# Kernel optimization log

Measured on AMD Instinct MI355X. Metric: run time of the kernel, lower is better.

The kernel has to match this reference:

```python
import jax, jax.numpy as jnp
import numpy as np

EPS = 1e-12  # torch F.normalize eps

def _normalize(x):
    n = jnp.sqrt(jnp.sum(x * x, axis=-1, keepdims=True))
    return x / jnp.maximum(n, EPS)

def bgs_extended(d6s):
    # d6s: [B, N, D, 3, 2] -> rotation [B, N, D, 3, 3] (columns b1,b2,b3)
    b1 = _normalize(d6s[..., :, 0])
    a2 = d6s[..., :, 1]
    dot = jnp.sum(b1 * a2, axis=-1, keepdims=True)
    b2 = _normalize(a2 - dot * b1)
    b3 = jnp.cross(b1, b2, axis=-1)
    return jnp.stack([b1, b2, b3], axis=-1)

def setup_inputs() -> dict:
    key = jax.random.key(0)
    k1, k2, k3, k4, k5 = jax.random.split(key, 5)
    B, N, D, F = 8, 8192, 64, 64
    X = jax.random.normal(k1, (B, N, D, 3), dtype=jnp.float32)
    J = jax.random.normal(k2, (B, N, D, 3, 2), dtype=jnp.float32)
    A = jax.random.normal(k3, (F, D), dtype=jnp.float32)
    Bm = jax.random.normal(k4, (F, D), dtype=jnp.float32)
    C = jax.random.normal(k5, (F, D), dtype=jnp.float32)
    return {"X": X, "J": J, "A": A, "Bm": Bm, "C": C}

def reference(X, J, A, Bm, C):
    R = bgs_extended(J)  # [B,N,D,3,3]
    # RT_i X = dot(column i of R, X) -> compute all three at once: [B,N,D,3]
    RTX = jnp.einsum('bndki,bndk->bndi', R, X)
    rt0, rt1, rt2 = RTX[..., 0:1], RTX[..., 1:2], RTX[..., 2:3]
    # get_rrtx(i, R, s) == R[..., :, i] * s
    a_term = R[..., :, 0] * rt0 + R[..., :, 1] * rt1
    b_term = R[..., :, 1] * rt0 - R[..., :, 0] * rt1
    c_term = R[..., :, 2] * rt2
    Y = (jnp.einsum('fe,bnei->bnfi', A, a_term)
         + jnp.einsum('fe,bnei->bnfi', Bm, b_term)
         + jnp.einsum('fe,bnei->bnfi', C, c_term))
    return Y
```

## Files before the change

kernel.cpp:

```cpp
#include <hip/hip_runtime.h>

typedef __bf16 bf16;
typedef bf16 bf16x8 __attribute__((ext_vector_type(8)));
typedef float f32x4 __attribute__((ext_vector_type(4)));
typedef unsigned int u32;

#define PTS 16
#define WREG 9216

__device__ __forceinline__ void gld_lds16(const void* g, void* l) {
    __builtin_amdgcn_global_load_lds(
        (const __attribute__((address_space(1))) u32*)g,
        (__attribute__((address_space(3))) u32*)l, 16, 0, 0);
}

__global__ __launch_bounds__(256, 4)
void affine_linear_fused(const float* __restrict__ X, const float* __restrict__ J,
                         const float* __restrict__ A, const float* __restrict__ Bm,
                         const float* __restrict__ C, float* __restrict__ Y)
{
    __shared__ __attribute__((aligned(128))) unsigned char lds[4 * WREG];

    const int tid  = threadIdx.x;
    const int wave = tid >> 6;
    const int lane = tid & 63;
    const int l16  = lane & 15;
    const int lq   = lane >> 4;
    const long bn0 = (long)blockIdx.x * PTS;

    unsigned char* wbase = &lds[wave * WREG];

    {
        const float* jg = J + (bn0 + wave * 4) * 64 * 6;
        const float* xg = X + (bn0 + wave * 4) * 64 * 3;
        #pragma unroll
        for (int t = 0; t < 6; ++t)
            gld_lds16(jg + t * 256 + lane * 4, wbase + t * 1024);
        #pragma unroll
        for (int t = 0; t < 3; ++t)
            gld_lds16(xg + t * 256 + lane * 4, wbase + 6144 + t * 1024);
    }

    const int f = wave * 16 + l16;
    bf16x8 wfrag[6];
    #pragma unroll
    for (int kk = 0; kk < 6; ++kk) {
        const float* src = (kk < 2) ? A : (kk < 4) ? Bm : C;
        const f32x4* p4 = (const f32x4*)(src + f * 64 + (kk & 1) * 32 + lq * 8);
        f32x4 lo = p4[0], hi = p4[1];
        bf16x8 w;
        w[0] = (bf16)lo[0]; w[1] = (bf16)lo[1]; w[2] = (bf16)lo[2]; w[3] = (bf16)lo[3];
        w[4] = (bf16)hi[0]; w[5] = (bf16)hi[1]; w[6] = (bf16)hi[2]; w[7] = (bf16)hi[3];
        wfrag[kk] = w;
    }

    __asm__ volatile("s_waitcnt vmcnt(0)" ::: "memory");

    const float* jlds = (const float*)wbase;
    const float* xlds = (const float*)(wbase + 6144);
    float jv[4][6], xv[4][3];
    #pragma unroll
    for (int q = 0; q < 4; ++q) {
        const float* jp = jlds + q * 384 + lane * 6;
        float2 ja = *(const float2*)(jp + 0);
        float2 jb = *(const float2*)(jp + 2);
        float2 jc = *(const float2*)(jp + 4);
        jv[q][0] = ja.x; jv[q][1] = ja.y;
        jv[q][2] = jb.x; jv[q][3] = jb.y;
        jv[q][4] = jc.x; jv[q][5] = jc.y;
        const float* xp = xlds + q * 192 + lane * 3;
        xv[q][0] = xp[0]; xv[q][1] = xp[1]; xv[q][2] = xp[2];
    }

    #pragma unroll
    for (int q = 0; q < 4; ++q) {
        float a1x = jv[q][0], a2x = jv[q][1];
        float a1y = jv[q][2], a2y = jv[q][3];
        float a1z = jv[q][4], a2z = jv[q][5];
        float xx = xv[q][0], xy = xv[q][1], xz = xv[q][2];

        float n1   = sqrtf(a1x*a1x + a1y*a1y + a1z*a1z);
        float inv1 = 1.0f / fmaxf(n1, 1e-12f);
        float b1x = a1x*inv1, b1y = a1y*inv1, b1z = a1z*inv1;
        float dot = b1x*a2x + b1y*a2y + b1z*a2z;
        float ux = a2x - dot*b1x, uy = a2y - dot*b1y, uz = a2z - dot*b1z;
        float n2   = sqrtf(ux*ux + uy*uy + uz*uz);
        float inv2 = 1.0f / fmaxf(n2, 1e-12f);
        float b2x = ux*inv2, b2y = uy*inv2, b2z = uz*inv2;
        float b3x = b1y*b2z - b1z*b2y;
        float b3y = b1z*b2x - b1x*b2z;
        float b3z = b1x*b2y - b1y*b2x;

        float rt0 = b1x*xx + b1y*xy + b1z*xz;
        float rt1 = b2x*xx + b2y*xy + b2z*xz;
        float rt2 = b3x*xx + b3y*xy + b3z*xz;

        float at0 = b1x*rt0 + b2x*rt1;
        float at1 = b1y*rt0 + b2y*rt1;
        float at2 = b1z*rt0 + b2z*rt1;
        float bt0 = b2x*rt0 - b1x*rt1;
        float bt1 = b2y*rt0 - b1y*rt1;
        float bt2 = b2z*rt0 - b1z*rt1;
        float ct0 = b3x*rt2, ct1 = b3y*rt2, ct2 = b3z*rt2;

        bf16* r0 = (bf16*)(wbase + (q*3 + 0) * 400);
        bf16* r1 = (bf16*)(wbase + (q*3 + 1) * 400);
        bf16* r2 = (bf16*)(wbase + (q*3 + 2) * 400);
        r0[lane] = (bf16)at0; r0[64+lane] = (bf16)bt0; r0[128+lane] = (bf16)ct0;
        r1[lane] = (bf16)at1; r1[64+lane] = (bf16)bt1; r1[128+lane] = (bf16)ct1;
        r2[lane] = (bf16)at2; r2[64+lane] = (bf16)bt2; r2[128+lane] = (bf16)ct2;
    }
    __syncthreads();

    f32x4 acc[3];
    #pragma unroll
    for (int mt = 0; mt < 3; ++mt) {
        int m  = mt * 16 + l16;
        int wv = m / 12;
        int r  = m - wv * 12;
        const unsigned char* arow = &lds[wv * WREG + r * 400] + lq * 16;
        f32x4 a = {0.f, 0.f, 0.f, 0.f};
        #pragma unroll
        for (int kk = 0; kk < 6; ++kk) {
            bf16x8 af = *(const bf16x8*)(arow + kk * 64);
            a = __builtin_amdgcn_mfma_f32_16x16x32_bf16(af, wfrag[kk], a, 0, 0, 0);
        }
        acc[mt] = a;
    }

    float* yw = (float*)(wbase + 4800);
    #pragma unroll
    for (int mt = 0; mt < 3; ++mt) {
        #pragma unroll
        for (int r = 0; r < 4; ++r) {
            int m  = mt * 16 + lq * 4 + r;
            int wv = m / 12;
            int rr = m - wv * 12;
            int q  = rr / 3;
            int i  = rr - q * 3;
            int p  = wv * 4 + q;
            yw[p * 48 + l16 * 3 + i] = acc[mt][r];
        }
    }

    const f32x4* ysrc = (const f32x4*)yw;
    #pragma unroll
    for (int v = 0; v < 3; ++v) {
        int vi = v * 64 + lane;
        int p  = vi / 12;
        int vo = vi - p * 12;
        f32x4* dst = (f32x4*)(Y + (bn0 + p) * 192 + wave * 48) + vo;
        *dst = ysrc[vi];
    }
}

extern "C" void kernel_launch(void* const* d_in, const int* in_sizes, int n_in,
                              void* d_out, int out_size, void* d_ws, size_t ws_size,
                              hipStream_t stream) {
    const float* X  = (const float*)d_in[0];
    const float* J  = (const float*)d_in[1];
    const float* A  = (const float*)d_in[2];
    const float* Bm = (const float*)d_in[3];
    const float* C  = (const float*)d_in[4];
    float* Y = (float*)d_out;

    const int points = in_sizes[0] / (64 * 3);
    const int blocks = points / PTS;
    affine_linear_fused<<<blocks, 256, 0, stream>>>(X, J, A, Bm, C, Y);
}
```

Baseline: 201.5 us.

## Shrink LDS footprint, load J directly to registers, stream weight fragments

J is now loaded straight from global memory into registers instead of being staged through LDS, so only X is staged and the per-wave LDS region shrinks from 9216 to 4800 bytes. Launch bounds rise from 4 to 7 blocks per CU to use the freed LDS and registers. Weight fragments are loaded one K-step ahead inside the MFMA loop instead of all six up front, which lowers register pressure. The normalisations use rsq on the squared norm instead of sqrt plus divide, a slight precision change. A second barrier is added so the output staging area can reuse the same LDS region.

```diff
diff --git a/kernel.cpp b/kernel.cpp
--- a/kernel.cpp
+++ b/kernel.cpp
@@ -6,7 +6,7 @@
 typedef unsigned int u32;
 
 #define PTS 16
-#define WREG 9216
+#define WREG 4800
 
 __device__ __forceinline__ void gld_lds16(const void* g, void* l) {
     __builtin_amdgcn_global_load_lds(
@@ -14,7 +14,7 @@
         (__attribute__((address_space(3))) u32*)l, 16, 0, 0);
 }
 
-__global__ __launch_bounds__(256, 4)
+__global__ __launch_bounds__(256, 7)
 void affine_linear_fused(const float* __restrict__ X, const float* __restrict__ J,
                          const float* __restrict__ A, const float* __restrict__ Bm,
                          const float* __restrict__ C, float* __restrict__ Y)
@@ -30,44 +30,29 @@
 
     unsigned char* wbase = &lds[wave * WREG];
 
-    {
-        const float* jg = J + (bn0 + wave * 4) * 64 * 6;
-        const float* xg = X + (bn0 + wave * 4) * 64 * 3;
-        #pragma unroll
-        for (int t = 0; t < 6; ++t)
-            gld_lds16(jg + t * 256 + lane * 4, wbase + t * 1024);
-        #pragma unroll
-        for (int t = 0; t < 3; ++t)
-            gld_lds16(xg + t * 256 + lane * 4, wbase + 6144 + t * 1024);
-    }
+    const float* xg = X + (bn0 + wave * 4) * 192;
+    #pragma unroll
+    for (int t = 0; t < 3; ++t)
+        gld_lds16(xg + t * 256 + lane * 4, wbase + t * 1024);
 
-    const int f = wave * 16 + l16;
-    bf16x8 wfrag[6];
+    const float* jg = J + (bn0 + wave * 4) * 384 + lane * 6;
+    float jv[4][6];
     #pragma unroll
-    for (int kk = 0; kk < 6; ++kk) {
-        const float* src = (kk < 2) ? A : (kk < 4) ? Bm : C;
-        const f32x4* p4 = (const f32x4*)(src + f * 64 + (kk & 1) * 32 + lq * 8);
-        f32x4 lo = p4[0], hi = p4[1];
-        bf16x8 w;
-        w[0] = (bf16)lo[0]; w[1] = (bf16)lo[1]; w[2] = (bf16)lo[2]; w[3] = (bf16)lo[3];
-        w[4] = (bf16)hi[0]; w[5] = (bf16)hi[1]; w[6] = (bf16)hi[2]; w[7] = (bf16)hi[3];
-        wfrag[kk] = w;
+    for (int q = 0; q < 4; ++q) {
+        float2 ja = *(const float2*)(jg + q * 384 + 0);
+        float2 jb = *(const float2*)(jg + q * 384 + 2);
+        float2 jc = *(const float2*)(jg + q * 384 + 4);
+        jv[q][0] = ja.x; jv[q][1] = ja.y;
+        jv[q][2] = jb.x; jv[q][3] = jb.y;
+        jv[q][4] = jc.x; jv[q][5] = jc.y;
     }
 
     __asm__ volatile("s_waitcnt vmcnt(0)" ::: "memory");
 
-    const float* jlds = (const float*)wbase;
-    const float* xlds = (const float*)(wbase + 6144);
-    float jv[4][6], xv[4][3];
+    const float* xlds = (const float*)wbase;
+    float xv[4][3];
     #pragma unroll
     for (int q = 0; q < 4; ++q) {
-        const float* jp = jlds + q * 384 + lane * 6;
-        float2 ja = *(const float2*)(jp + 0);
-        float2 jb = *(const float2*)(jp + 2);
-        float2 jc = *(const float2*)(jp + 4);
-        jv[q][0] = ja.x; jv[q][1] = ja.y;
-        jv[q][2] = jb.x; jv[q][3] = jb.y;
-        jv[q][4] = jc.x; jv[q][5] = jc.y;
         const float* xp = xlds + q * 192 + lane * 3;
         xv[q][0] = xp[0]; xv[q][1] = xp[1]; xv[q][2] = xp[2];
     }
@@ -79,13 +64,13 @@
         float a1z = jv[q][4], a2z = jv[q][5];
         float xx = xv[q][0], xy = xv[q][1], xz = xv[q][2];
 
-        float n1   = sqrtf(a1x*a1x + a1y*a1y + a1z*a1z);
-        float inv1 = 1.0f / fmaxf(n1, 1e-12f);
+        float n1sq = a1x*a1x + a1y*a1y + a1z*a1z;
+        float inv1 = __builtin_amdgcn_rsqf(fmaxf(n1sq, 1e-24f));
         float b1x = a1x*inv1, b1y = a1y*inv1, b1z = a1z*inv1;
         float dot = b1x*a2x + b1y*a2y + b1z*a2z;
         float ux = a2x - dot*b1x, uy = a2y - dot*b1y, uz = a2z - dot*b1z;
-        float n2   = sqrtf(ux*ux + uy*uy + uz*uz);
-        float inv2 = 1.0f / fmaxf(n2, 1e-12f);
+        float n2sq = ux*ux + uy*uy + uz*uz;
+        float inv2 = __builtin_amdgcn_rsqf(fmaxf(n2sq, 1e-24f));
         float b2x = ux*inv2, b2y = uy*inv2, b2z = uz*inv2;
         float b3x = b1y*b2z - b1z*b2y;
         float b3y = b1z*b2x - b1x*b2z;
@@ -110,25 +95,49 @@
         r1[lane] = (bf16)at1; r1[64+lane] = (bf16)bt1; r1[128+lane] = (bf16)ct1;
         r2[lane] = (bf16)at2; r2[64+lane] = (bf16)bt2; r2[128+lane] = (bf16)ct2;
     }
+
+    const int f = wave * 16 + l16;
+    const float* wp0 = A + f * 64 + lq * 8;
+    f32x4 wlo = *(const f32x4*)wp0;
+    f32x4 whi = *(const f32x4*)(wp0 + 4);
+
     __syncthreads();
 
-    f32x4 acc[3];
+    const unsigned char* arow[3];
     #pragma unroll
     for (int mt = 0; mt < 3; ++mt) {
         int m  = mt * 16 + l16;
         int wv = m / 12;
         int r  = m - wv * 12;
-        const unsigned char* arow = &lds[wv * WREG + r * 400] + lq * 16;
-        f32x4 a = {0.f, 0.f, 0.f, 0.f};
+        arow[mt] = &lds[wv * WREG + r * 400] + lq * 16;
+    }
+    f32x4 acc[3];
+    #pragma unroll
+    for (int mt = 0; mt < 3; ++mt) acc[mt] = (f32x4){0.f, 0.f, 0.f, 0.f};
+
+    #pragma unroll
+    for (int kk = 0; kk < 6; ++kk) {
+        f32x4 nlo = wlo, nhi = whi;
+        if (kk < 5) {
+            const float* src = (kk + 1 < 2) ? A : (kk + 1 < 4) ? Bm : C;
+            const float* p = src + f * 64 + ((kk + 1) & 1) * 32 + lq * 8;
+            nlo = *(const f32x4*)p;
+            nhi = *(const f32x4*)(p + 4);
+        }
+        bf16x8 w;
+        w[0] = (bf16)wlo[0]; w[1] = (bf16)wlo[1]; w[2] = (bf16)wlo[2]; w[3] = (bf16)wlo[3];
+        w[4] = (bf16)whi[0]; w[5] = (bf16)whi[1]; w[6] = (bf16)whi[2]; w[7] = (bf16)whi[3];
         #pragma unroll
-        for (int kk = 0; kk < 6; ++kk) {
-            bf16x8 af = *(const bf16x8*)(arow + kk * 64);
-            a = __builtin_amdgcn_mfma_f32_16x16x32_bf16(af, wfrag[kk], a, 0, 0, 0);
+        for (int mt = 0; mt < 3; ++mt) {
+            bf16x8 af = *(const bf16x8*)(arow[mt] + kk * 64);
+            acc[mt] = __builtin_amdgcn_mfma_f32_16x16x32_bf16(af, w, acc[mt], 0, 0, 0);
         }
-        acc[mt] = a;
+        wlo = nlo; whi = nhi;
     }
 
-    float* yw = (float*)(wbase + 4800);
+    __syncthreads();
+
+    float* yw = (float*)wbase;
     #pragma unroll
     for (int mt = 0; mt < 3; ++mt) {
         #pragma unroll
```

Result: slower. 206.9 us (+2.7%).
